# Optimization experiments

Measured on AMD Instinct MI355X. Metric: run time of the kernel, lower is better.

The kernel has to match this reference:

```python
import jax, jax.numpy as jnp
import numpy as np

B, S, H, HKV, D = 1, 1024, 32, 8, 128
HID = H * D
GROUPS = H // HKV
ALPHA_K, ALPHA_V = 0.5, 0.5
GAMMA_MIN, GAMMA_MAX = 0.5, 2.0
ETA_MIN, ETA_MAX = 0.5, 2.0
BETA_BIAS, BIAS_CAP = 1.0, 5.0
BETA_POST = 0.5
ROPE_THETA = 10000.0


def setup_inputs() -> dict:
    key = jax.random.key(0)
    ks = jax.random.split(key, 9)
    hidden_states = jax.random.normal(ks[0], (B, S, HID), jnp.float32) * 0.02
    # additive causal mask (LLaMA-style, large negative above diagonal)
    causal = jnp.tril(jnp.ones((S, S), dtype=bool))
    attention_mask = jnp.where(causal, 0.0, -1e9).astype(jnp.float32)[None, None]
    position_ids = jnp.arange(S, dtype=jnp.int32)[None]
    sq = 1.0 / np.sqrt(HID)
    Wq = jax.random.normal(ks[1], (HID, HID), jnp.float32) * sq
    Wk = jax.random.normal(ks[2], (HKV * D, HID), jnp.float32) * sq
    Wv = jax.random.normal(ks[3], (HKV * D, HID), jnp.float32) * sq
    Wo = jax.random.normal(ks[4], (HID, HID), jnp.float32) * sq
    prior = jax.random.uniform(ks[5], (S,), jnp.float32)  # per-key-position prior, in [0,1)
    head_mask_l1 = (jax.random.uniform(ks[6], (H,)) > 0.5).astype(jnp.float32)
    head_mask_l2 = (jax.random.uniform(ks[7], (H,)) > 0.5).astype(jnp.float32)
    return {"hidden_states": hidden_states, "attention_mask": attention_mask,
            "position_ids": position_ids, "Wq": Wq, "Wk": Wk, "Wv": Wv, "Wo": Wo,
            "prior": prior, "head_mask_l1": head_mask_l1, "head_mask_l2": head_mask_l2}


def _rope(position_ids):
    inv_freq = 1.0 / (ROPE_THETA ** (jnp.arange(0, D, 2, dtype=jnp.float32) / D))
    freqs = position_ids.astype(jnp.float32)[..., None] * inv_freq  # [B,S,D/2]
    emb = jnp.concatenate([freqs, freqs], axis=-1)                  # [B,S,D]
    return jnp.cos(emb)[:, None], jnp.sin(emb)[:, None]             # [B,1,S,D]


def _rotate_half(x):
    x1, x2 = x[..., : D // 2], x[..., D // 2:]
    return jnp.concatenate([-x2, x1], axis=-1)


def reference(hidden_states, attention_mask, position_ids, Wq, Wk, Wv, Wo,
              prior, head_mask_l1, head_mask_l2):
    b, s, _ = hidden_states.shape
    # projections (Linear without bias: x @ W.T)
    q = (hidden_states @ Wq.T).reshape(b, s, H, D).transpose(0, 2, 1, 3)     # [B,H,S,D]
    k = (hidden_states @ Wk.T).reshape(b, s, HKV, D).transpose(0, 2, 1, 3)   # [B,Hkv,S,D]
    v = (hidden_states @ Wv.T).reshape(b, s, HKV, D).transpose(0, 2, 1, 3)
    cos, sin = _rope(position_ids)
    q = q * cos + _rotate_half(q) * sin
    k = k * cos + _rotate_half(k) * sin
    # repeat_kv: expand KV heads to match query heads (GQA)
    k = jnp.repeat(k, GROUPS, axis=1)  # [B,H,S,D]
    v = jnp.repeat(v, GROUPS, axis=1)
    # level4_scale: per-key-position multiplicative scaling of K and V
    gamma = jnp.clip(1.0 + ALPHA_K * prior, GAMMA_MIN, GAMMA_MAX)  # [S]
    eta = jnp.clip(1.0 + ALPHA_V * prior, ETA_MIN, ETA_MAX)
    k = k * gamma[None, None, :, None]
    v = v * eta[None, None, :, None]
    # attention logits
    attn = jnp.einsum('bhqd,bhkd->bhqk', q, k) / np.sqrt(D)
    # level1_bias: capped additive bias on logits, blended per-head
    bias = jnp.clip(BETA_BIAS * prior, -BIAS_CAP, BIAS_CAP)        # [S] over key dim
    steered = attn + bias[None, None, None, :]
    attn = attn + (steered - attn) * head_mask_l1[None, :, None, None]
    # causal mask
    attn = attn + attention_mask
    probs = jax.nn.softmax(attn.astype(jnp.float32), axis=-1)
    # level2_post: post-softmax rescale + renormalize, blended per-head
    sp = probs * (1.0 + BETA_POST * prior)[None, None, None, :]
    sp = sp / jnp.sum(sp, axis=-1, keepdims=True)
    probs = probs + (sp - probs) * head_mask_l2[None, :, None, None]
    out = jnp.einsum('bhqk,bhkd->bhqd', probs, v)                  # [B,H,S,D]
    out = out.transpose(0, 2, 1, 3).reshape(b, s, HID)
    return out @ Wo.T
```

## Files before the change

kernel.cpp:

```cpp
#include <hip/hip_runtime.h>
#include <math.h>

#define S_LEN 1024
#define HID_DIM 4096
#define NH 32
#define NKV 8
#define DH 128

typedef __attribute__((ext_vector_type(8))) short sh8;
typedef __attribute__((ext_vector_type(4))) short sh4;
typedef __attribute__((ext_vector_type(4))) float f4;

__device__ __forceinline__ unsigned short f2bf(float x) {
    union { float f; unsigned int u; } v; v.f = x;
    unsigned int r = v.u + 0x7FFFu + ((v.u >> 16) & 1u);
    return (unsigned short)(r >> 16);
}

__device__ __forceinline__ void gl_lds16(const unsigned short* g, unsigned short* l) {
    __builtin_amdgcn_global_load_lds(
        (const __attribute__((address_space(1))) unsigned int*)g,
        (__attribute__((address_space(3))) unsigned int*)l, 16, 0, 0);
}


__global__ void cvt_hw(const float* __restrict__ hidden, const float* __restrict__ Wq,
                       const float* __restrict__ Wk, const float* __restrict__ Wv,
                       unsigned short* __restrict__ hbf, unsigned short* __restrict__ wbuf)
{
    const int idx = blockIdx.x * 256 + threadIdx.x;
    const int NH4 = (S_LEN * HID_DIM) / 4;
    float4 v;
    sh4* dst;
    if (idx < NH4) {
        v = ((const float4*)hidden)[idx];
        dst = (sh4*)hbf + idx;
    } else {
        const int j = idx - NH4;
        const int row = j >> 10;
        if (row < 4096)      v = ((const float4*)Wq)[j];
        else if (row < 5120) v = ((const float4*)Wk)[j - 4096 * 1024];
        else                 v = ((const float4*)Wv)[j - 5120 * 1024];
        dst = (sh4*)wbuf + j;
    }
    sh4 o;
    o.x = (short)f2bf(v.x); o.y = (short)f2bf(v.y);
    o.z = (short)f2bf(v.z); o.w = (short)f2bf(v.w);
    *dst = o;
}

__global__ void cvt_wo(const float* __restrict__ Wo, unsigned short* __restrict__ wbuf)
{
    const int idx = blockIdx.x * 256 + threadIdx.x;
    const float4 v = ((const float4*)Wo)[idx];
    sh4 o;
    o.x = (short)f2bf(v.x); o.y = (short)f2bf(v.y);
    o.z = (short)f2bf(v.z); o.w = (short)f2bf(v.w);
    ((sh4*)wbuf)[idx] = o;
}

__global__ __launch_bounds__(256)
void gemm_t(const unsigned short* __restrict__ A, const unsigned short* __restrict__ B,
            float* __restrict__ C, int K, int ldc)
{
    __shared__ __attribute__((aligned(16))) unsigned short sA[2][64 * 32];
    __shared__ __attribute__((aligned(16))) unsigned short sB[2][128 * 32];

    const int tid  = threadIdx.x;
    const int wave = tid >> 6;
    const int lane = tid & 63;
    const int l15  = lane & 15;
    const int quad = lane >> 4;
    const int m0   = blockIdx.y * 64;
    const int n0   = blockIdx.x * 128;
    const int wm   = (wave >> 1) * 32;
    const int wn   = (wave & 1) * 64;

    const int sslot = (lane & 7) ^ ((lane >> 3) & 7);
    const int srow  = 2 * (lane >> 3) + (sslot >> 2);
    const int scol  = (sslot & 3) * 8;

    const unsigned short* Ag  = A + (size_t)(m0 + 16 * wave + srow) * K + scol;
    const unsigned short* Bg1 = B + (size_t)(n0 + 16 * wave + srow) * K + scol;
    const unsigned short* Bg2 = B + (size_t)(n0 + 64 + 16 * wave + srow) * K + scol;

    f4 acc[2][4];
#pragma unroll
    for (int i = 0; i < 2; i++)
#pragma unroll
        for (int j = 0; j < 4; j++)
            acc[i][j] = f4{0.0f, 0.0f, 0.0f, 0.0f};

    const int rphys = ((((l15 & 1) << 2) + quad) ^ (l15 >> 1)) * 8;

    gl_lds16(Ag,  &sA[0][wave * 512]);
    gl_lds16(Bg1, &sB[0][wave * 512]);
    gl_lds16(Bg2, &sB[0][2048 + wave * 512]);

    for (int k0 = 0; k0 < K; k0 += 32) {
        const int cur = (k0 >> 5) & 1;
        __syncthreads();
        const int k1 = k0 + 32;
        if (k1 < K) {
            gl_lds16(Ag + k1,  &sA[cur ^ 1][wave * 512]);
            gl_lds16(Bg1 + k1, &sB[cur ^ 1][wave * 512]);
            gl_lds16(Bg2 + k1, &sB[cur ^ 1][2048 + wave * 512]);
        }

        sh8 af[2], bf[4];
#pragma unroll
        for (int i = 0; i < 2; i++)
            af[i] = *(const sh8*)(&sA[cur][((wm + i * 16 + l15) >> 1) * 64 + rphys]);
#pragma unroll
        for (int j = 0; j < 4; j++)
            bf[j] = *(const sh8*)(&sB[cur][((wn + j * 16 + l15) >> 1) * 64 + rphys]);
#pragma unroll
        for (int i = 0; i < 2; i++)
#pragma unroll
            for (int j = 0; j < 4; j++)
                acc[i][j] = __builtin_amdgcn_mfma_f32_16x16x32_bf16(af[i], bf[j], acc[i][j], 0, 0, 0);
    }

#pragma unroll
    for (int i = 0; i < 2; i++) {
        const int mrow = m0 + wm + i * 16 + quad * 4;
#pragma unroll
        for (int j = 0; j < 4; j++) {
            const int ncol = n0 + wn + j * 16 + l15;
#pragma unroll
            for (int r = 0; r < 4; r++)
                C[(size_t)(mrow + r) * ldc + ncol] = acc[i][j][r];
        }
    }
}

__global__ void prep2(const float* __restrict__ qkv, const int* __restrict__ pos_ids,
                      const float* __restrict__ prior,
                      unsigned short* __restrict__ Qb, unsigned short* __restrict__ Kb,
                      unsigned short* __restrict__ Vt, float* __restrict__ addvT)
{
    const int idx = blockIdx.x * blockDim.x + threadIdx.x;
    const int NQ = S_LEN * 40 * 64;
    const int NV = S_LEN * NKV * DH;
    if (idx < NQ) {
        const int s   = idx / (40 * 64);
        const int rem = idx % (40 * 64);
        const int hh  = rem >> 6;
        const int i   = rem & 63;
        const float pos  = (float)pos_ids[s];
        const float invf = exp2f(-13.287712379549449f * (i * 0.015625f));
        const float ph = pos * invf;
        const float c = cosf(ph), sn = sinf(ph);
        if (hh < NH) {
            const float* base = qkv + (size_t)s * 6144 + hh * 128;
            const float x1 = base[i], x2 = base[i + 64];
            const float sc = 0.08838834764831845f * 1.4426950408889634f;
            unsigned short* q = Qb + ((size_t)hh * S_LEN + s) * DH;
            q[i]      = f2bf((x1 * c - x2 * sn) * sc);
            q[i + 64] = f2bf((x2 * c + x1 * sn) * sc);
        } else {
            const int kvh = hh - NH;
            const float* base = qkv + (size_t)s * 6144 + 4096 + kvh * 128;
            const float p = prior[s];
            const float gamma = fminf(fmaxf(1.0f + 0.5f * p, 0.5f), 2.0f);
            const float x1 = base[i], x2 = base[i + 64];
            unsigned short* kp = Kb + ((size_t)kvh * S_LEN + s) * DH;
            kp[i]      = f2bf((x1 * c - x2 * sn) * gamma);
            kp[i + 64] = f2bf((x2 * c + x1 * sn) * gamma);
        }
    } else if (idx < NQ + NV) {
        const int j = idx - NQ;
        const int s   = j / (NKV * DH);
        const int rem = j % (NKV * DH);
        const int kvh = rem >> 7;
        const int d   = rem & 127;
        const float p = prior[s];
        const float eta = fminf(fmaxf(1.0f + 0.5f * p, 0.5f), 2.0f);
        const float val = qkv[(size_t)s * 6144 + 5120 + kvh * 128 + d] * eta;
        Vt[((size_t)kvh * DH + d) * S_LEN + s] = f2bf(val);
    } else {
        const int j2 = idx - NQ - NV;
        if (j2 < 4 * S_LEN) {
            const int c = j2 >> 10;
            const int s = j2 & 1023;
            const float p = prior[s];
            const float bias = fminf(fmaxf(p, -5.0f), 5.0f);
            float v = 0.0f;
            if (c & 1) v += bias;
            if (c & 2) v += log1pf(0.5f * p);
            addvT[j2] = v * 1.4426950408889634f;
        }
    }
}

__global__ __launch_bounds__(256)
void attn5(const unsigned short* __restrict__ Qb, const unsigned short* __restrict__ Kb,
           const unsigned short* __restrict__ Vt, const float* __restrict__ addvT,
           const float* __restrict__ hm1, const float* __restrict__ hm2,
           unsigned short* __restrict__ ctx)
{
    __shared__ __attribute__((aligned(16))) unsigned short sK[32 * 128];
    __shared__ __attribute__((aligned(16))) unsigned short sV[128 * 32];
    __shared__ __attribute__((aligned(16))) short sP[4][16 * 40];

    const int h    = blockIdx.x;
    const int qb   = (gridDim.y - 1) - blockIdx.y;
    const int tid  = threadIdx.x;
    const int wave = tid >> 6;
    const int lane = tid & 63;
    const int l15  = lane & 15;
    const int quad = lane >> 4;
    const int q0   = qb * 64 + wave * 16;
    const int kvh  = h >> 2;
    const int combo = (hm1[h] > 0.5f ? 1 : 0) + (hm2[h] > 0.5f ? 2 : 0);
    const float* av = addvT + combo * S_LEN;

    const unsigned short* ksrcE = Kb + ((size_t)kvh * S_LEN + (lane >> 4)) * DH
                                  + (((lane & 15) ^ (lane >> 4)) * 8);
    const unsigned short* ksrcO = Kb + ((size_t)kvh * S_LEN + (lane >> 4)) * DH
                                  + (((lane & 15) ^ (4 + (lane >> 4))) * 8);
    const unsigned short* vsrc0 = Vt + ((size_t)kvh * DH + (lane >> 2)) * S_LEN
                                  + (((lane & 3) ^ ((lane >> 2) & 3)) * 8);

    sh8 qf[4];
    {
        const unsigned short* qbase = Qb + ((size_t)h * S_LEN + q0 + l15) * DH + quad * 8;
#pragma unroll
        for (int kc = 0; kc < 4; kc++)
            qf[kc] = *(const sh8*)(qbase + kc * 32);
    }

    f4 O[8];
#pragma unroll
    for (int dt = 0; dt < 8; dt++) O[dt] = f4{0.0f, 0.0f, 0.0f, 0.0f};
    float lrun[4] = {0.0f, 0.0f, 0.0f, 0.0f};

    short* pl = &sP[wave][0];
    const int sw = l15 & 7;
    const int sv = l15 & 3;
    const int nch = 2 * qb + 2;

    for (int c = 0; c < nch; c++) {
        const int k0 = c * 32;
        __syncthreads();
        if (wave < 2) {
#pragma unroll
            for (int j = 0; j < 4; j++) {
                const int i = wave * 4 + j;
                const unsigned short* src = (j & 1) ? ksrcO : ksrcE;
                gl_lds16(src + (size_t)(k0 + 4 * i) * DH, &sK[i * 512]);
            }
        } else {
#pragma unroll
            for (int j = 0; j < 4; j++) {
                const int i = (wave - 2) * 4 + j;
                gl_lds16(vsrc0 + (size_t)(16 * i) * S_LEN + k0, &sV[i * 512]);
            }
        }
        __syncthreads();

#pragma unroll
        for (int t = 0; t < 2; t++) {
            f4 a = f4{0.0f, 0.0f, 0.0f, 0.0f};
#pragma unroll
            for (int kc = 0; kc < 4; kc++) {
                const sh8 kfr = *(const sh8*)(&sK[(t * 16 + l15) * 128 + ((kc * 4 + quad) ^ sw) * 8]);
                a = __builtin_amdgcn_mfma_f32_16x16x32_bf16(qf[kc], kfr, a, 0, 0, 0);
            }
            const int key = k0 + t * 16 + l15;
            const float ad = av[key];
#pragma unroll
            for (int r = 0; r < 4; r++) {
                const int qrow = q0 + quad * 4 + r;
                float ex = exp2f(a[r] + ad);
                ex = (key <= qrow) ? ex : 0.0f;
                lrun[r] += ex;
                pl[(quad * 4 + r) * 40 + t * 16 + l15] = (short)f2bf(ex);
            }
        }
        asm volatile("s_waitcnt lgkmcnt(0)" ::: "memory");
        const sh8 ap = *(const sh8*)(&pl[l15 * 40 + quad * 8]);
#pragma unroll
        for (int dt = 0; dt < 8; dt++) {
            const sh8 vfr = *(const sh8*)(&sV[(dt * 16 + l15) * 32 + (quad ^ sv) * 8]);
            O[dt] = __builtin_amdgcn_mfma_f32_16x16x32_bf16(ap, vfr, O[dt], 0, 0, 0);
        }
    }

#pragma unroll
    for (int r = 0; r < 4; r++) {
        float l = lrun[r];
        l += __shfl_xor(l, 1); l += __shfl_xor(l, 2);
        l += __shfl_xor(l, 4); l += __shfl_xor(l, 8);
        const float inv = 1.0f / l;
        const int row = q0 + quad * 4 + r;
        unsigned short* cp = ctx + (size_t)row * HID_DIM + h * DH;
#pragma unroll
        for (int dt = 0; dt < 8; dt++)
            cp[dt * 16 + l15] = f2bf(O[dt][r] * inv);
    }
}


#define LDSW 40

__global__ __launch_bounds__(256)
void gemm_bt(const float* __restrict__ A,
             const float* __restrict__ B0, const float* __restrict__ B1,
             const float* __restrict__ B2, int n_b1, int n_b2,
             float* __restrict__ C, int M, int N, int K, int ldc)
{
    __shared__ __attribute__((aligned(16))) short sA[128 * LDSW];
    __shared__ __attribute__((aligned(16))) short sB[128 * LDSW];
    const int tid  = threadIdx.x;
    const int m0   = blockIdx.y * 128;
    const int n0   = blockIdx.x * 128;
    const float* Bp = B0; int nloc = n0;
    if (n0 >= n_b2)      { Bp = B2; nloc = n0 - n_b2; }
    else if (n0 >= n_b1) { Bp = B1; nloc = n0 - n_b1; }
    const int wave = tid >> 6, lane = tid & 63;
    const int l15 = lane & 15, quad = lane >> 4;
    const int wm = (wave >> 1) * 64, wn = (wave & 1) * 64;
    const int rb = tid >> 3, c4 = (tid & 7) * 4;
    f4 acc[4][4];
#pragma unroll
    for (int i = 0; i < 4; i++)
#pragma unroll
        for (int j = 0; j < 4; j++) acc[i][j] = f4{0.0f, 0.0f, 0.0f, 0.0f};
    for (int k0 = 0; k0 < K; k0 += 32) {
        __syncthreads();
#pragma unroll
        for (int i = 0; i < 4; i++) {
            const int row = rb + 32 * i;
            const float4 va = *(const float4*)(A  + (size_t)(m0 + row) * K + k0 + c4);
            const float4 vb = *(const float4*)(Bp + (size_t)(nloc + row) * K + k0 + c4);
            sh4 sa, sb;
            sa.x = (short)f2bf(va.x); sa.y = (short)f2bf(va.y);
            sa.z = (short)f2bf(va.z); sa.w = (short)f2bf(va.w);
            sb.x = (short)f2bf(vb.x); sb.y = (short)f2bf(vb.y);
            sb.z = (short)f2bf(vb.z); sb.w = (short)f2bf(vb.w);
            *(sh4*)(&sA[row * LDSW + c4]) = sa;
            *(sh4*)(&sB[row * LDSW + c4]) = sb;
        }
        __syncthreads();
        sh8 af[4], bf[4];
#pragma unroll
        for (int i = 0; i < 4; i++) af[i] = *(const sh8*)(&sA[(wm + i * 16 + l15) * LDSW + quad * 8]);
#pragma unroll
        for (int j = 0; j < 4; j++) bf[j] = *(const sh8*)(&sB[(wn + j * 16 + l15) * LDSW + quad * 8]);
#pragma unroll
        for (int i = 0; i < 4; i++)
#pragma unroll
            for (int j = 0; j < 4; j++)
                acc[i][j] = __builtin_amdgcn_mfma_f32_16x16x32_bf16(af[i], bf[j], acc[i][j], 0, 0, 0);
    }
#pragma unroll
    for (int i = 0; i < 4; i++) {
        const int mrow = m0 + wm + i * 16 + quad * 4;
#pragma unroll
        for (int j = 0; j < 4; j++) {
            const int ncol = n0 + wn + j * 16 + l15;
#pragma unroll
            for (int r = 0; r < 4; r++)
                C[(size_t)(mrow + r) * ldc + ncol] = acc[i][j][r];
        }
    }
}

__global__ void prep_rope(const float* __restrict__ qkv, const int* __restrict__ pos_ids,
                          const float* __restrict__ prior,
                          unsigned short* __restrict__ Qb, unsigned short* __restrict__ Kb,
                          unsigned short* __restrict__ Vt)
{
    const int idx = blockIdx.x * blockDim.x + threadIdx.x;
    const int NQ = S_LEN * 40 * 64;
    if (idx < NQ) {
        const int s = idx / (40 * 64);
        const int rem = idx % (40 * 64);
        const int hh = rem >> 6, i = rem & 63;
        const float pos = (float)pos_ids[s];
        const float invf = exp2f(-13.287712379549449f * (i * 0.015625f));
        const float ph = pos * invf;
        const float c = cosf(ph), sn = sinf(ph);
        if (hh < NH) {
            const float* base = qkv + (size_t)s * 6144 + hh * 128;
            const float x1 = base[i], x2 = base[i + 64];
            const float sc = 0.08838834764831845f;
            unsigned short* q = Qb + ((size_t)hh * S_LEN + s) * DH;
            q[i] = f2bf((x1 * c - x2 * sn) * sc);
            q[i + 64] = f2bf((x2 * c + x1 * sn) * sc);
        } else {
            const int kvh = hh - NH;
            const float* base = qkv + (size_t)s * 6144 + 4096 + kvh * 128;
            const float p = prior[s];
            const float gamma = fminf(fmaxf(1.0f + 0.5f * p, 0.5f), 2.0f);
            const float x1 = base[i], x2 = base[i + 64];
            unsigned short* kp = Kb + ((size_t)kvh * S_LEN + s) * DH;
            kp[i] = f2bf((x1 * c - x2 * sn) * gamma);
            kp[i + 64] = f2bf((x2 * c + x1 * sn) * gamma);
        }
    } else {
        const int j = idx - NQ;
        if (j < S_LEN * NKV * DH) {
            const int s = j / (NKV * DH);
            const int rem = j % (NKV * DH);
            const int kvh = rem >> 7, d = rem & 127;
            const float p = prior[s];
            const float eta = fminf(fmaxf(1.0f + 0.5f * p, 0.5f), 2.0f);
            const float val = qkv[(size_t)s * 6144 + 5120 + kvh * 128 + d] * eta;
            Vt[((size_t)kvh * DH + d) * S_LEN + s] = f2bf(val);
        }
    }
}

__global__ __launch_bounds__(256)
void attn_kernel(const unsigned short* __restrict__ Qb, const unsigned short* __restrict__ Kb,
                 const unsigned short* __restrict__ Vt, const float* __restrict__ prior,
                 const float* __restrict__ hm1, const float* __restrict__ hm2,
                 float* __restrict__ ctx)
{
    __shared__ __attribute__((aligned(16))) short p_lds[4][16 * LDSW];
    const int h = blockIdx.x, qb = blockIdx.y;
    const int wave = threadIdx.x >> 6, lane = threadIdx.x & 63;
    const int l15 = lane & 15, quad = lane >> 4;
    const int q0 = qb * 64 + wave * 16;
    const int kvh = h >> 2;
    const float m1 = hm1[h], m2 = hm2[h];
    const float NEG = -3.0e38f;
    sh8 qf[4];
    {
        const unsigned short* qbase = Qb + ((size_t)h * S_LEN + q0 + l15) * DH + quad * 8;
#pragma unroll
        for (int kc = 0; kc < 4; kc++) qf[kc] = *(const sh8*)(qbase + kc * 32);
    }
    f4 O[8];
#pragma unroll
    for (int dt = 0; dt < 8; dt++) O[dt] = f4{0.0f, 0.0f, 0.0f, 0.0f};
    float mrun[4], lrun[4];
#pragma unroll
    for (int r = 0; r < 4; r++) { mrun[r] = NEG; lrun[r] = 0.0f; }
    short* pl = &p_lds[wave][0];
    const int qmax = q0 + 15;
    for (int key0 = 0; key0 <= qmax; key0 += 32) {
        float sc[2][4];
#pragma unroll
        for (int t = 0; t < 2; t++) {
            const int kt = key0 + t * 16;
            const unsigned short* kb = Kb + ((size_t)kvh * S_LEN + kt + l15) * DH + quad * 8;
            f4 a = f4{0.0f, 0.0f, 0.0f, 0.0f};
#pragma unroll
            for (int kc = 0; kc < 4; kc++) {
                const sh8 bfr = *(const sh8*)(kb + kc * 32);
                a = __builtin_amdgcn_mfma_f32_16x16x32_bf16(qf[kc], bfr, a, 0, 0, 0);
            }
            const int key = kt + l15;
            const float p = prior[key];
            const float bias = fminf(fmaxf(p, -5.0f), 5.0f);
            const float addv = m1 * bias + m2 * logf(1.0f + 0.5f * p);
#pragma unroll
            for (int r = 0; r < 4; r++) {
                const int qrow = q0 + quad * 4 + r;
                sc[t][r] = (key <= qrow) ? (a[r] + addv) : NEG;
            }
        }
        float cm[4], mnew[4], alpha[4], rs[4];
#pragma unroll
        for (int r = 0; r < 4; r++) {
            cm[r] = fmaxf(sc[0][r], sc[1][r]);
            cm[r] = fmaxf(cm[r], __shfl_xor(cm[r], 1));
            cm[r] = fmaxf(cm[r], __shfl_xor(cm[r], 2));
            cm[r] = fmaxf(cm[r], __shfl_xor(cm[r], 4));
            cm[r] = fmaxf(cm[r], __shfl_xor(cm[r], 8));
            mnew[r] = fmaxf(mrun[r], cm[r]);
            alpha[r] = expf(mrun[r] - mnew[r]);
        }
        float e[2][4];
#pragma unroll
        for (int t = 0; t < 2; t++)
#pragma unroll
            for (int r = 0; r < 4; r++) e[t][r] = expf(sc[t][r] - mnew[r]);
#pragma unroll
        for (int r = 0; r < 4; r++) {
            rs[r] = e[0][r] + e[1][r];
            rs[r] += __shfl_xor(rs[r], 1); rs[r] += __shfl_xor(rs[r], 2);
            rs[r] += __shfl_xor(rs[r], 4); rs[r] += __shfl_xor(rs[r], 8);
            lrun[r] = lrun[r] * alpha[r] + rs[r];
            mrun[r] = mnew[r];
        }
#pragma unroll
        for (int dt = 0; dt < 8; dt++)
#pragma unroll
            for (int r = 0; r < 4; r++) O[dt][r] *= alpha[r];
#pragma unroll
        for (int t = 0; t < 2; t++)
#pragma unroll
            for (int r = 0; r < 4; r++)
                pl[(quad * 4 + r) * LDSW + t * 16 + l15] = (short)f2bf(e[t][r]);
        asm volatile("s_waitcnt lgkmcnt(0)" ::: "memory");
        const sh8 ap = *(const sh8*)(&pl[l15 * LDSW + quad * 8]);
        const unsigned short* vb = Vt + ((size_t)kvh * DH + l15) * S_LEN + key0 + quad * 8;
#pragma unroll
        for (int dt = 0; dt < 8; dt++) {
            const sh8 bfv = *(const sh8*)(vb + (size_t)dt * 16 * S_LEN);
            O[dt] = __builtin_amdgcn_mfma_f32_16x16x32_bf16(ap, bfv, O[dt], 0, 0, 0);
        }
    }
#pragma unroll
    for (int r = 0; r < 4; r++) {
        const float inv = 1.0f / lrun[r];
        const int row = q0 + quad * 4 + r;
        float* cp = ctx + (size_t)row * HID_DIM + h * DH;
#pragma unroll
        for (int dt = 0; dt < 8; dt++) cp[dt * 16 + l15] = O[dt][r] * inv;
    }
}


extern "C" void kernel_launch(void* const* d_in, const int* in_sizes, int n_in,
                              void* d_out, int out_size, void* d_ws, size_t ws_size,
                              hipStream_t stream)
{
    const float* hidden  = (const float*)d_in[0];
    const int*   pos_ids = (const int*)d_in[2];
    const float* Wq = (const float*)d_in[3];
    const float* Wk = (const float*)d_in[4];
    const float* Wv = (const float*)d_in[5];
    const float* Wo = (const float*)d_in[6];
    const float* prior = (const float*)d_in[7];
    const float* hm1 = (const float*)d_in[8];
    const float* hm2 = (const float*)d_in[9];
    float* out = (float*)d_out;
    char* ws = (char*)d_ws;

    const size_t FAST_NEED = 96485376ull;
    if (ws_size >= FAST_NEED) {
        unsigned short* Wbuf = (unsigned short*)ws;
        unsigned short* Cbf  = (unsigned short*)(ws + 33554432);
        unsigned short* Hbf  = (unsigned short*)(ws + 50331648);
        float*          qkv  = (float*)(ws + 58720256);
        unsigned short* Qb   = (unsigned short*)(ws + 83886080);
        unsigned short* Kb   = (unsigned short*)(ws + 92274688);
        unsigned short* Vt   = (unsigned short*)(ws + 94371840);
        float*          addv = (float*)(ws + 96468992);

        cvt_hw<<<28672, 256, 0, stream>>>(hidden, Wq, Wk, Wv, Hbf, Wbuf);
        gemm_t<<<dim3(48, 16), 256, 0, stream>>>(Hbf, Wbuf, qkv, 4096, 6144);
        prep2<<<14352, 256, 0, stream>>>(qkv, pos_ids, prior, Qb, Kb, Vt, addv);
        cvt_wo<<<16384, 256, 0, stream>>>(Wo, Wbuf);
        attn5<<<dim3(32, 16), 256, 0, stream>>>(Qb, Kb, Vt, addv, hm1, hm2, Cbf);
        gemm_t<<<dim3(32, 16), 256, 0, stream>>>(Cbf, Wbuf, out, 4096, 4096);
    } else {
        float*          qkv = (float*)ws;
        float*          ctx = (float*)(ws + 25165824);
        unsigned short* Qb  = (unsigned short*)(ws + 41943040);
        unsigned short* Kb  = (unsigned short*)(ws + 50331648);
        unsigned short* Vt  = (unsigned short*)(ws + 52428800);
        gemm_bt<<<dim3(48, 8), 256, 0, stream>>>(hidden, Wq, Wk, Wv, 4096, 5120,
                                                 qkv, 1024, 6144, 4096, 6144);
        prep_rope<<<14336, 256, 0, stream>>>(qkv, pos_ids, prior, Qb, Kb, Vt);
        attn_kernel<<<dim3(32, 16), 256, 0, stream>>>(Qb, Kb, Vt, prior, hm1, hm2, ctx);
        gemm_bt<<<dim3(32, 8), 256, 0, stream>>>(ctx, Wo, Wo, Wo, 1 << 30, 1 << 30,
                                                 out, 1024, 4096, 4096, 4096);
    }
}
```

Measured before the change: 407.7 us.

## Deepen GEMM K-step, double-buffer attention K/V, fuse Wo conversion into prep

The GEMM now loads two 32-wide K slices per stage, so each barrier covers a 64-wide K step and there are half as many __syncthreads. The attention kernel double-buffers its K/V tiles in LDS, prefetching the next chunk while the current one is computed. This removes one barrier per chunk, and s_setprio raises wave priority around the MFMA blocks. The separate Wo fp32-to-bf16 conversion launch is folded into prep2, saving a kernel launch. The cost is doubled LDS use in both kernels, which may lower occupancy.

```diff
diff --git a/kernel.cpp b/kernel.cpp
--- a/kernel.cpp
+++ b/kernel.cpp
@@ -49,22 +49,12 @@
     *dst = o;
 }
 
-__global__ void cvt_wo(const float* __restrict__ Wo, unsigned short* __restrict__ wbuf)
-{
-    const int idx = blockIdx.x * 256 + threadIdx.x;
-    const float4 v = ((const float4*)Wo)[idx];
-    sh4 o;
-    o.x = (short)f2bf(v.x); o.y = (short)f2bf(v.y);
-    o.z = (short)f2bf(v.z); o.w = (short)f2bf(v.w);
-    ((sh4*)wbuf)[idx] = o;
-}
-
 __global__ __launch_bounds__(256)
 void gemm_t(const unsigned short* __restrict__ A, const unsigned short* __restrict__ B,
             float* __restrict__ C, int K, int ldc)
 {
-    __shared__ __attribute__((aligned(16))) unsigned short sA[2][64 * 32];
-    __shared__ __attribute__((aligned(16))) unsigned short sB[2][128 * 32];
+    __shared__ __attribute__((aligned(16))) unsigned short sA[2][2][64 * 32];
+    __shared__ __attribute__((aligned(16))) unsigned short sB[2][2][128 * 32];
 
     const int tid  = threadIdx.x;
     const int wave = tid >> 6;
@@ -93,32 +83,41 @@
 
     const int rphys = ((((l15 & 1) << 2) + quad) ^ (l15 >> 1)) * 8;
 
-    gl_lds16(Ag,  &sA[0][wave * 512]);
-    gl_lds16(Bg1, &sB[0][wave * 512]);
-    gl_lds16(Bg2, &sB[0][2048 + wave * 512]);
-
-    for (int k0 = 0; k0 < K; k0 += 32) {
-        const int cur = (k0 >> 5) & 1;
+#pragma unroll
+    for (int s = 0; s < 2; s++) {
+        gl_lds16(Ag + 32 * s,  &sA[0][s][wave * 512]);
+        gl_lds16(Bg1 + 32 * s, &sB[0][s][wave * 512]);
+        gl_lds16(Bg2 + 32 * s, &sB[0][s][2048 + wave * 512]);
+    }
+
+    for (int k0 = 0; k0 < K; k0 += 64) {
+        const int cur = (k0 >> 6) & 1;
         __syncthreads();
-        const int k1 = k0 + 32;
+        const int k1 = k0 + 64;
         if (k1 < K) {
-            gl_lds16(Ag + k1,  &sA[cur ^ 1][wave * 512]);
-            gl_lds16(Bg1 + k1, &sB[cur ^ 1][wave * 512]);
-            gl_lds16(Bg2 + k1, &sB[cur ^ 1][2048 + wave * 512]);
-        }
-
-        sh8 af[2], bf[4];
-#pragma unroll
-        for (int i = 0; i < 2; i++)
-            af[i] = *(const sh8*)(&sA[cur][((wm + i * 16 + l15) >> 1) * 64 + rphys]);
-#pragma unroll
-        for (int j = 0; j < 4; j++)
-            bf[j] = *(const sh8*)(&sB[cur][((wn + j * 16 + l15) >> 1) * 64 + rphys]);
-#pragma unroll
-        for (int i = 0; i < 2; i++)
+#pragma unroll
+            for (int s = 0; s < 2; s++) {
+                gl_lds16(Ag + k1 + 32 * s,  &sA[cur ^ 1][s][wave * 512]);
+                gl_lds16(Bg1 + k1 + 32 * s, &sB[cur ^ 1][s][wave * 512]);
+                gl_lds16(Bg2 + k1 + 32 * s, &sB[cur ^ 1][s][2048 + wave * 512]);
+            }
+        }
+
+#pragma unroll
+        for (int s = 0; s < 2; s++) {
+            sh8 af[2], bf[4];
+#pragma unroll
+            for (int i = 0; i < 2; i++)
+                af[i] = *(const sh8*)(&sA[cur][s][((wm + i * 16 + l15) >> 1) * 64 + rphys]);
 #pragma unroll
             for (int j = 0; j < 4; j++)
-                acc[i][j] = __builtin_amdgcn_mfma_f32_16x16x32_bf16(af[i], bf[j], acc[i][j], 0, 0, 0);
+                bf[j] = *(const sh8*)(&sB[cur][s][((wn + j * 16 + l15) >> 1) * 64 + rphys]);
+#pragma unroll
+            for (int i = 0; i < 2; i++)
+#pragma unroll
+                for (int j = 0; j < 4; j++)
+                    acc[i][j] = __builtin_amdgcn_mfma_f32_16x16x32_bf16(af[i], bf[j], acc[i][j], 0, 0, 0);
+        }
     }
 
 #pragma unroll
@@ -136,8 +135,10 @@
 
 __global__ void prep2(const float* __restrict__ qkv, const int* __restrict__ pos_ids,
                       const float* __restrict__ prior,
+                      const float* __restrict__ Wo,
                       unsigned short* __restrict__ Qb, unsigned short* __restrict__ Kb,
-                      unsigned short* __restrict__ Vt, float* __restrict__ addvT)
+                      unsigned short* __restrict__ Vt, float* __restrict__ addvT,
+                      unsigned short* __restrict__ Wob)
 {
     const int idx = blockIdx.x * blockDim.x + threadIdx.x;
     const int NQ = S_LEN * 40 * 64;
@@ -189,6 +190,15 @@
             if (c & 1) v += bias;
             if (c & 2) v += log1pf(0.5f * p);
             addvT[j2] = v * 1.4426950408889634f;
+        } else {
+            const int j3 = j2 - 4 * S_LEN;
+            if (j3 < (HID_DIM * HID_DIM) / 4) {
+                const float4 v = ((const float4*)Wo)[j3];
+                sh4 o;
+                o.x = (short)f2bf(v.x); o.y = (short)f2bf(v.y);
+                o.z = (short)f2bf(v.z); o.w = (short)f2bf(v.w);
+                ((sh4*)Wob)[j3] = o;
+            }
         }
     }
 }
@@ -199,8 +209,8 @@
            const float* __restrict__ hm1, const float* __restrict__ hm2,
            unsigned short* __restrict__ ctx)
 {
-    __shared__ __attribute__((aligned(16))) unsigned short sK[32 * 128];
-    __shared__ __attribute__((aligned(16))) unsigned short sV[128 * 32];
+    __shared__ __attribute__((aligned(16))) unsigned short sK[2][32 * 128];
+    __shared__ __attribute__((aligned(16))) unsigned short sV[2][128 * 32];
     __shared__ __attribute__((aligned(16))) short sP[4][16 * 40];
 
     const int h    = blockIdx.x;
@@ -222,6 +232,24 @@
     const unsigned short* vsrc0 = Vt + ((size_t)kvh * DH + (lane >> 2)) * S_LEN
                                   + (((lane & 3) ^ ((lane >> 2) & 3)) * 8);
 
+    auto stage = [&](int c, int buf) {
+        const int k0 = c * 32;
+        if (wave < 2) {
+#pragma unroll
+            for (int j = 0; j < 4; j++) {
+                const int i = wave * 4 + j;
+                const unsigned short* src = (j & 1) ? ksrcO : ksrcE;
+                gl_lds16(src + (size_t)(k0 + 4 * i) * DH, &sK[buf][i * 512]);
+            }
+        } else {
+#pragma unroll
+            for (int j = 0; j < 4; j++) {
+                const int i = (wave - 2) * 4 + j;
+                gl_lds16(vsrc0 + (size_t)(16 * i) * S_LEN + k0, &sV[buf][i * 512]);
+            }
+        }
+    };
+
     sh8 qf[4];
     {
         const unsigned short* qbase = Qb + ((size_t)h * S_LEN + q0 + l15) * DH + quad * 8;
@@ -240,33 +268,24 @@
     const int sv = l15 & 3;
     const int nch = 2 * qb + 2;
 
+    stage(0, 0);
+
     for (int c = 0; c < nch; c++) {
+        const int cur = c & 1;
         const int k0 = c * 32;
         __syncthreads();
-        if (wave < 2) {
-#pragma unroll
-            for (int j = 0; j < 4; j++) {
-                const int i = wave * 4 + j;
-                const unsigned short* src = (j & 1) ? ksrcO : ksrcE;
-                gl_lds16(src + (size_t)(k0 + 4 * i) * DH, &sK[i * 512]);
-            }
-        } else {
-#pragma unroll
-            for (int j = 0; j < 4; j++) {
-                const int i = (wave - 2) * 4 + j;
-                gl_lds16(vsrc0 + (size_t)(16 * i) * S_LEN + k0, &sV[i * 512]);
-            }
-        }
-        __syncthreads();
+        if (c + 1 < nch) stage(c + 1, cur ^ 1);
 
 #pragma unroll
         for (int t = 0; t < 2; t++) {
             f4 a = f4{0.0f, 0.0f, 0.0f, 0.0f};
+            __builtin_amdgcn_s_setprio(1);
 #pragma unroll
             for (int kc = 0; kc < 4; kc++) {
-                const sh8 kfr = *(const sh8*)(&sK[(t * 16 + l15) * 128 + ((kc * 4 + quad) ^ sw) * 8]);
+                const sh8 kfr = *(const sh8*)(&sK[cur][(t * 16 + l15) * 128 + ((kc * 4 + quad) ^ sw) * 8]);
                 a = __builtin_amdgcn_mfma_f32_16x16x32_bf16(qf[kc], kfr, a, 0, 0, 0);
             }
+            __builtin_amdgcn_s_setprio(0);
             const int key = k0 + t * 16 + l15;
             const float ad = av[key];
 #pragma unroll
@@ -280,11 +299,13 @@
         }
         asm volatile("s_waitcnt lgkmcnt(0)" ::: "memory");
         const sh8 ap = *(const sh8*)(&pl[l15 * 40 + quad * 8]);
+        __builtin_amdgcn_s_setprio(1);
 #pragma unroll
         for (int dt = 0; dt < 8; dt++) {
-            const sh8 vfr = *(const sh8*)(&sV[(dt * 16 + l15) * 32 + (quad ^ sv) * 8]);
+            const sh8 vfr = *(const sh8*)(&sV[cur][(dt * 16 + l15) * 32 + (quad ^ sv) * 8]);
             O[dt] = __builtin_amdgcn_mfma_f32_16x16x32_bf16(ap, vfr, O[dt], 0, 0, 0);
         }
+        __builtin_amdgcn_s_setprio(0);
     }
 
 #pragma unroll
@@ -545,8 +566,7 @@
 
         cvt_hw<<<28672, 256, 0, stream>>>(hidden, Wq, Wk, Wv, Hbf, Wbuf);
         gemm_t<<<dim3(48, 16), 256, 0, stream>>>(Hbf, Wbuf, qkv, 4096, 6144);
-        prep2<<<14352, 256, 0, stream>>>(qkv, pos_ids, prior, Qb, Kb, Vt, addv);
-        cvt_wo<<<16384, 256, 0, stream>>>(Wo, Wbuf);
+        prep2<<<30736, 256, 0, stream>>>(qkv, pos_ids, prior, Wo, Qb, Kb, Vt, addv, Wbuf);
         attn5<<<dim3(32, 16), 256, 0, stream>>>(Qb, Kb, Vt, addv, hm1, hm2, Cbf);
         gemm_t<<<dim3(32, 16), 256, 0, stream>>>(Cbf, Wbuf, out, 4096, 4096);
     } else {
```

Result: faster. 373.4 us (-8.4%).
